# Performance work log

Hardware: AMD Instinct MI355X
Metric: run time of the kernel (lower is better)

The kernel has to match this reference:

```python
import jax, jax.numpy as jnp
import numpy as np

ROPE_THETA = 10000.0
NUM_HEADS = 16


def _apply_rope(t, positions):
    # t: [B, H, S, dh]; positions: [S] int
    dh = t.shape[-1]
    inv_freq = 1.0 / (ROPE_THETA ** (jnp.arange(0, dh, 2, dtype=jnp.float32) / dh))  # [dh/2]
    ang = positions.astype(jnp.float32)[:, None] * inv_freq[None, :]  # [S, dh/2]
    cos = jnp.cos(ang)[None, None]  # [1,1,S,dh/2]
    sin = jnp.sin(ang)[None, None]
    t1 = t[..., 0::2]
    t2 = t[..., 1::2]
    r1 = t1 * cos - t2 * sin
    r2 = t1 * sin + t2 * cos
    # interleave back: (r1_0, r2_0, r1_1, r2_1, ...)
    return jnp.stack([r1, r2], axis=-1).reshape(t.shape)


def setup_inputs() -> dict:
    key = jax.random.key(0)
    ks = jax.random.split(key, 5)
    B, S, D = 4, 2048, 1024
    sigma = np.sqrt(2.0 / (D + D))
    return {
        "x": jax.random.normal(ks[0], (B, S, D), dtype=jnp.float32),
        "WQ": jax.random.normal(ks[1], (D, D), dtype=jnp.float32) * sigma,
        "WK": jax.random.normal(ks[2], (D, D), dtype=jnp.float32) * sigma,
        "WV": jax.random.normal(ks[3], (D, D), dtype=jnp.float32) * sigma,
        "WO": jax.random.normal(ks[4], (D, D), dtype=jnp.float32) * sigma,
        "token_positions": jnp.arange(S, dtype=jnp.int32),
    }


def reference(x, WQ, WK, WV, WO, token_positions):
    B, S, D = x.shape
    H = NUM_HEADS
    dh = D // H

    def proj(W):
        # x @ W.T, then split heads -> [B, H, S, dh]
        return jnp.einsum('bsd,ed->bse', x, W).reshape(B, S, H, dh).transpose(0, 2, 1, 3)

    Q = _apply_rope(proj(WQ), token_positions)
    K = _apply_rope(proj(WK), token_positions)
    V = proj(WV)

    scale = 1.0 / jnp.sqrt(jnp.asarray(dh, dtype=x.dtype))
    scores = jnp.einsum('bhqd,bhkd->bhqk', Q, K) * scale  # [B,H,S,S]
    causal = jnp.tril(jnp.ones((S, S), dtype=bool))
    scores = jnp.where(causal[None, None], scores, jnp.asarray(-jnp.inf, dtype=scores.dtype))
    attn = jax.nn.softmax(scores, axis=-1)
    out = jnp.einsum('bhqk,bhkd->bhqd', attn, V)  # [B,H,S,dh]
    out = out.transpose(0, 2, 1, 3).reshape(B, S, D)
    return out @ WO.T
```

## Files before the change

kernel.cpp:

```cpp
#include <hip/hip_runtime.h>
#include <hip/hip_bf16.h>
#include <math.h>

constexpr int NB   = 4;
constexpr int SEQ  = 2048;
constexpr int DM   = 1024;
constexpr int NH   = 16;
constexpr int DH2  = 64;
constexpr int NROWS = NB * SEQ;

typedef __attribute__((ext_vector_type(8))) short bf16x8;
typedef __attribute__((ext_vector_type(4))) short bf16x4;
typedef __attribute__((ext_vector_type(4))) float f32x4;

__device__ __forceinline__ unsigned short f2bf(float f) {
  __hip_bfloat16 h = __float2bfloat16(f);
  return *reinterpret_cast<unsigned short*>(&h);
}

__device__ __forceinline__ f32x4 mfma16(bf16x8 a, bf16x8 b, f32x4 c) {
  return __builtin_amdgcn_mfma_f32_16x16x32_bf16(a, b, c, 0, 0, 0);
}

__device__ __forceinline__ f32x4 mfma16k16(bf16x4 a, bf16x4 b, f32x4 c) {
  asm("v_mfma_f32_16x16x16_bf16 %0, %1, %2, %0" : "+v"(c) : "v"(a), "v"(b));
  return c;
}

__device__ __forceinline__ void gload_lds16(const void* g, void* l) {
  __builtin_amdgcn_global_load_lds(
      (const __attribute__((address_space(1))) void*)g,
      (__attribute__((address_space(3))) void*)l, 16, 0, 0);
}

__global__ void cast_kernel(const float* __restrict__ in,
                            unsigned short* __restrict__ out, int n4) {
  int i = blockIdx.x * blockDim.x + threadIdx.x;
  int stride = gridDim.x * blockDim.x;
  for (int idx = i; idx < n4; idx += stride) {
    float4 v = reinterpret_cast<const float4*>(in)[idx];
    ushort4 o;
    o.x = f2bf(v.x); o.y = f2bf(v.y); o.z = f2bf(v.z); o.w = f2bf(v.w);
    reinterpret_cast<ushort4*>(out)[idx] = o;
  }
}

__global__ void cast4_kernel(const float* __restrict__ w0, const float* __restrict__ w1,
                             const float* __restrict__ w2, const float* __restrict__ w3,
                             unsigned short* __restrict__ out) {
  constexpr int N4 = DM * DM / 4;
  int idx = blockIdx.x * blockDim.x + threadIdx.x;
  if (idx >= N4) return;
  const float* ins[4] = {w0, w1, w2, w3};
#pragma unroll
  for (int wi = 0; wi < 4; ++wi) {
    float4 v = reinterpret_cast<const float4*>(ins[wi])[idx];
    ushort4 o;
    o.x = f2bf(v.x); o.y = f2bf(v.y); o.z = f2bf(v.z); o.w = f2bf(v.w);
    reinterpret_cast<ushort4*>(out + (size_t)wi * DM * DM)[idx] = o;
  }
}

__global__ void rope_table_kernel(float2* __restrict__ tab, const int* __restrict__ pos) {
  int idx = blockIdx.x * blockDim.x + threadIdx.x;
  if (idx >= SEQ * 32) return;
  int s = idx >> 5, i = idx & 31;
  float inv = powf(10000.0f, -(float)i * (1.0f / 32.0f));
  float ang = (float)pos[s] * inv;
  tab[idx] = make_float2(cosf(ang), sinf(ang));
}

template<int MODE>
__global__ __launch_bounds__(256)
void gemm_bt(const unsigned short* __restrict__ Ag,
             const unsigned short* __restrict__ Bg,
             void* __restrict__ Cout,
             const float2* __restrict__ tab)
{
  constexpr int K = DM;
  __shared__ unsigned short As[128 * 32];
  __shared__ unsigned short Bs[128 * 32];
  const int tid = threadIdx.x;
  const int w = tid >> 6, lane = tid & 63;
  const int wr = w >> 1, wc = w & 1;
  const int r = lane & 15, g = lane >> 4;
  const int rowTile = blockIdx.x, colTile = blockIdx.y;
  const unsigned short* Abase = Ag + (size_t)rowTile * 128 * K;
  const unsigned short* Bbase = Bg + (size_t)colTile * 128 * K;

  f32x4 acc[4][4];
#pragma unroll
  for (int m = 0; m < 4; ++m)
#pragma unroll
    for (int n = 0; n < 4; ++n) acc[m][n] = f32x4{0.f, 0.f, 0.f, 0.f};

  const int e0 = w * 1024 + lane * 8;

  for (int k0 = 0; k0 < K; k0 += 32) {
#pragma unroll
    for (int c = 0; c < 2; ++c) {
      int e = e0 + c * 512;
      int trow = e >> 5, tcol = e & 31;
      gload_lds16(Abase + (size_t)trow * K + k0 + tcol, As + (w * 2 + c) * 512);
      gload_lds16(Bbase + (size_t)trow * K + k0 + tcol, Bs + (w * 2 + c) * 512);
    }
    __syncthreads();
    bf16x8 a[4], b[4];
#pragma unroll
    for (int m = 0; m < 4; ++m)
      a[m] = *reinterpret_cast<const bf16x8*>(As + (wr * 64 + m * 16 + r) * 32 + g * 8);
#pragma unroll
    for (int n = 0; n < 4; ++n)
      b[n] = *reinterpret_cast<const bf16x8*>(Bs + (wc * 64 + n * 16 + r) * 32 + g * 8);
#pragma unroll
    for (int m = 0; m < 4; ++m)
#pragma unroll
      for (int n = 0; n < 4; ++n)
        acc[m][n] = mfma16(a[m], b[n], acc[m][n]);
    __syncthreads();
  }

  const int row0 = rowTile * 128 + wr * 64;
  const int col0 = colTile * 128 + wc * 64;
  if constexpr (MODE == 0) {
    float* C = reinterpret_cast<float*>(Cout);
#pragma unroll
    for (int m = 0; m < 4; ++m)
#pragma unroll
      for (int n = 0; n < 4; ++n)
#pragma unroll
        for (int j = 0; j < 4; ++j) {
          int rr = row0 + m * 16 + g * 4 + j;
          int cc = col0 + n * 16 + r;
          C[(size_t)rr * DM + cc] = acc[m][n][j];
        }
  } else {
    unsigned short* Ob = reinterpret_cast<unsigned short*>(Cout);
#pragma unroll
    for (int m = 0; m < 4; ++m)
#pragma unroll
      for (int n = 0; n < 4; ++n)
#pragma unroll
        for (int j = 0; j < 4; ++j) {
          int rr = row0 + m * 16 + g * 4 + j;
          int ee = col0 + n * 16 + r;
          float val = acc[m][n][j];
          if constexpr (MODE == 1) {
            float partner = __shfl_xor(val, 1);
            int dd = ee & 63;
            int sr = rr & (SEQ - 1);
            float2 cs = tab[sr * 32 + (dd >> 1)];
            val = val * cs.x + (((ee & 1) == 0) ? -partner : partner) * cs.y;
          }
          int bb = rr >> 11;
          int sr2 = rr & (SEQ - 1);
          int h = ee >> 6, d = ee & 63;
          Ob[((size_t)(bb * NH + h) * SEQ + sr2) * DH2 + d] = f2bf(val);
        }
  }
}

__global__ __launch_bounds__(256)
void flash_attn(const unsigned short* __restrict__ Qb,
                const unsigned short* __restrict__ Kb,
                const unsigned short* __restrict__ Vb,
                unsigned short* __restrict__ AO)
{
  constexpr int VST = 68;
  __shared__ unsigned short Vt[2][64 * VST];
  const int tid = threadIdx.x;
  const int w = tid >> 6, lane = tid & 63;
  const int r = lane & 15, g = lane >> 4;
  const int pr = blockIdx.x;
  const int bh = blockIdx.y;
  const unsigned short* Qh = Qb + (size_t)bh * SEQ * DH2;
  const unsigned short* Kh = Kb + (size_t)bh * SEQ * DH2;
  const unsigned short* Vh = Vb + (size_t)bh * SEQ * DH2;
  const int bb = bh >> 4, h = bh & 15;
  const int vd  = (lane & 7) * 8;
  const int vkv = w * 16 + (lane >> 3) * 2;
  const float C = 0.18033688f;
  const float M0 = 11.5415603f;
  const float NEG_INF = -__builtin_inff();

  for (int ctx = 0; ctx < 2; ++ctx) {
    const int qt = ctx ? pr : (15 - pr);
    const int q0w = qt * 128 + w * 32;
    const int nT  = 2 * qt + 2;
    const int myT = 2 * qt + 1 + (w >> 1);

    bf16x8 qf[2][2];
#pragma unroll
    for (int mq = 0; mq < 2; ++mq)
#pragma unroll
      for (int kk = 0; kk < 2; ++kk)
        qf[mq][kk] = *reinterpret_cast<const bf16x8*>(
            Qh + (size_t)(q0w + mq * 16 + r) * DH2 + kk * 32 + g * 8);

    bf16x8 kc[2][4], kn[2][4];
#pragma unroll
    for (int kk = 0; kk < 2; ++kk)
#pragma unroll
      for (int nk = 0; nk < 4; ++nk)
        kc[kk][nk] = *reinterpret_cast<const bf16x8*>(
            Kh + (size_t)(nk * 16 + r) * DH2 + kk * 32 + g * 8);

    {
      uint4 a0 = *reinterpret_cast<const uint4*>(Vh + (size_t)vkv * DH2 + vd);
      uint4 a1 = *reinterpret_cast<const uint4*>(Vh + (size_t)(vkv + 1) * DH2 + vd);
      const unsigned int* d0 = reinterpret_cast<const unsigned int*>(&a0);
      const unsigned int* d1 = reinterpret_cast<const unsigned int*>(&a1);
#pragma unroll
      for (int k2 = 0; k2 < 4; ++k2) {
        *reinterpret_cast<unsigned int*>(&Vt[0][(vd + 2 * k2) * VST + vkv]) =
            __builtin_amdgcn_perm(d1[k2], d0[k2], 0x05040100u);
        *reinterpret_cast<unsigned int*>(&Vt[0][(vd + 2 * k2 + 1) * VST + vkv]) =
            __builtin_amdgcn_perm(d1[k2], d0[k2], 0x07060302u);
      }
    }
    __syncthreads();

    f32x4 oacc[2][4];
    float l_part[2];
#pragma unroll
    for (int mq = 0; mq < 2; ++mq) {
#pragma unroll
      for (int nd = 0; nd < 4; ++nd) oacc[mq][nd] = f32x4{0.f, 0.f, 0.f, 0.f};
      l_part[mq] = 0.f;
    }

    uint4 va0, va1;
    for (int t = 0; t < nT; ++t) {
      const int cur = t & 1;
      const int tn = (t + 1 < nT) ? (t + 1) : t;
      const size_t kv0n = (size_t)tn * 64;

#pragma unroll
      for (int kk = 0; kk < 2; ++kk)
#pragma unroll
        for (int nk = 0; nk < 4; ++nk)
          kn[kk][nk] = *reinterpret_cast<const bf16x8*>(
              Kh + (kv0n + nk * 16 + r) * DH2 + kk * 32 + g * 8);
      va0 = *reinterpret_cast<const uint4*>(Vh + (kv0n + vkv) * DH2 + vd);
      va1 = *reinterpret_cast<const uint4*>(Vh + (kv0n + vkv + 1) * DH2 + vd);

      if (t < myT) {
        const int kv0 = t * 64;
        f32x4 sacc[2][4];
#pragma unroll
        for (int mq = 0; mq < 2; ++mq)
#pragma unroll
          for (int nk = 0; nk < 4; ++nk) sacc[mq][nk] = f32x4{0.f, 0.f, 0.f, 0.f};
        __builtin_amdgcn_s_setprio(1);
#pragma unroll
        for (int kk = 0; kk < 2; ++kk)
#pragma unroll
          for (int mq = 0; mq < 2; ++mq)
#pragma unroll
            for (int nk = 0; nk < 4; ++nk)
              sacc[mq][nk] = mfma16(kc[kk][nk], qf[mq][kk], sacc[mq][nk]);
        __builtin_amdgcn_s_setprio(0);

        if (t == myT - 1) {
#pragma unroll
          for (int mq = 0; mq < 2; ++mq) {
            const int qg = q0w + mq * 16 + r;
#pragma unroll
            for (int nk = 0; nk < 4; ++nk)
#pragma unroll
              for (int j = 0; j < 4; ++j) {
                int kg = kv0 + nk * 16 + g * 4 + j;
                if (kg > qg) sacc[mq][nk][j] = NEG_INF;
              }
          }
        }

        bf16x4 pa[2][4];
#pragma unroll
        for (int mq = 0; mq < 2; ++mq) {
          float ls = 0.f;
#pragma unroll
          for (int nk = 0; nk < 4; ++nk) {
            float p0 = __builtin_amdgcn_exp2f(fmaf(sacc[mq][nk][0], C, -M0));
            float p1 = __builtin_amdgcn_exp2f(fmaf(sacc[mq][nk][1], C, -M0));
            float p2 = __builtin_amdgcn_exp2f(fmaf(sacc[mq][nk][2], C, -M0));
            float p3 = __builtin_amdgcn_exp2f(fmaf(sacc[mq][nk][3], C, -M0));
            ls += (p0 + p1) + (p2 + p3);
            pa[mq][nk] = bf16x4{(short)f2bf(p0), (short)f2bf(p1),
                                (short)f2bf(p2), (short)f2bf(p3)};
          }
          l_part[mq] += ls;
        }

        __builtin_amdgcn_s_setprio(1);
#pragma unroll
        for (int nd = 0; nd < 4; ++nd) {
          bf16x4 vb[4];
#pragma unroll
          for (int nk = 0; nk < 4; ++nk)
            vb[nk] = *reinterpret_cast<const bf16x4*>(
                &Vt[cur][(nd * 16 + r) * VST + nk * 16 + 4 * g]);
#pragma unroll
          for (int mq = 0; mq < 2; ++mq)
#pragma unroll
            for (int nk = 0; nk < 4; ++nk)
              oacc[mq][nd] = mfma16k16(pa[mq][nk], vb[nk], oacc[mq][nd]);
        }
        __builtin_amdgcn_s_setprio(0);
      }

      {
        const unsigned int* d0 = reinterpret_cast<const unsigned int*>(&va0);
        const unsigned int* d1 = reinterpret_cast<const unsigned int*>(&va1);
#pragma unroll
        for (int k2 = 0; k2 < 4; ++k2) {
          *reinterpret_cast<unsigned int*>(&Vt[cur ^ 1][(vd + 2 * k2) * VST + vkv]) =
              __builtin_amdgcn_perm(d1[k2], d0[k2], 0x05040100u);
          *reinterpret_cast<unsigned int*>(&Vt[cur ^ 1][(vd + 2 * k2 + 1) * VST + vkv]) =
              __builtin_amdgcn_perm(d1[k2], d0[k2], 0x07060302u);
        }
      }
#pragma unroll
      for (int kk = 0; kk < 2; ++kk)
#pragma unroll
        for (int nk = 0; nk < 4; ++nk) kc[kk][nk] = kn[kk][nk];
      __syncthreads();
    }

#pragma unroll
    for (int mq = 0; mq < 2; ++mq) {
      float l = l_part[mq];
      l += __shfl_xor(l, 16);
      l += __shfl_xor(l, 32);
#pragma unroll
      for (int j = 0; j < 4; ++j) {
        float inv = 1.0f / __shfl(l, g * 4 + j);
        int srow = q0w + mq * 16 + g * 4 + j;
#pragma unroll
        for (int nd = 0; nd < 4; ++nd) {
          int d = nd * 16 + r;
          AO[(size_t)(bb * SEQ + srow) * DM + h * DH2 + d] = f2bf(oacc[mq][nd][j] * inv);
        }
      }
    }
  }
}

extern "C" void kernel_launch(void* const* d_in, const int* in_sizes, int n_in,
                              void* d_out, int out_size, void* d_ws, size_t ws_size,
                              hipStream_t stream) {
  const float* x  = (const float*)d_in[0];
  const float* WQ = (const float*)d_in[1];
  const float* WK = (const float*)d_in[2];
  const float* WV = (const float*)d_in[3];
  const float* WO = (const float*)d_in[4];
  const int* pos  = (const int*)d_in[5];

  char* ws = (char*)d_ws;
  unsigned short* xb  = (unsigned short*)(ws + 0);
  unsigned short* wqb = (unsigned short*)(ws + (16u << 20));
  unsigned short* wkb = (unsigned short*)(ws + (18u << 20));
  unsigned short* wvb = (unsigned short*)(ws + (20u << 20));
  unsigned short* wob = (unsigned short*)(ws + (22u << 20));
  unsigned short* Qb  = (unsigned short*)(ws + (24u << 20));
  unsigned short* Kb  = (unsigned short*)(ws + (40u << 20));
  unsigned short* Vb  = (unsigned short*)(ws + (56u << 20));
  unsigned short* AO  = (unsigned short*)(ws + (72u << 20));
  float2* tab = (float2*)(ws + (88u << 20));

  cast_kernel<<<2048, 256, 0, stream>>>(x, xb, NROWS * DM / 4);
  cast4_kernel<<<DM * DM / 4 / 256, 256, 0, stream>>>(WQ, WK, WV, WO, wqb);
  rope_table_kernel<<<(SEQ * 32 + 255) / 256, 256, 0, stream>>>(tab, pos);

  dim3 gproj(NROWS / 128, DM / 128);
  gemm_bt<1><<<gproj, 256, 0, stream>>>(xb, wqb, (void*)Qb, tab);
  gemm_bt<1><<<gproj, 256, 0, stream>>>(xb, wkb, (void*)Kb, tab);
  gemm_bt<2><<<gproj, 256, 0, stream>>>(xb, wvb, (void*)Vb, nullptr);
  flash_attn<<<dim3(8, NB * NH), 256, 0, stream>>>(Qb, Kb, Vb, AO);
  gemm_bt<0><<<gproj, 256, 0, stream>>>(AO, wob, d_out, nullptr);
}
```

Baseline: 204.2 us.

## Stage K tiles in shared memory via direct global-to-LDS loads

Instead of each wave loading the full K tile from global memory into registers (redundantly across 4 waves), the block cooperatively loads each K tile into a double-buffered, XOR-swizzled shared buffer using direct global-to-LDS loads, then each wave reads its fragments from LDS. This cuts redundant global/L2 traffic and register pressure from the kc/kn prefetch arrays. It adds LDS reads per iteration, more shared memory per block, and relies on the existing barrier for the async load to complete.

```diff
diff --git a/kernel.cpp b/kernel.cpp
--- a/kernel.cpp
+++ b/kernel.cpp
@@ -167,6 +167,7 @@
                 unsigned short* __restrict__ AO)
 {
   constexpr int VST = 68;
+  __shared__ unsigned short Kl[2 * 64 * 64];
   __shared__ unsigned short Vt[2][64 * VST];
   const int tid = threadIdx.x;
   const int w = tid >> 6, lane = tid & 63;
@@ -183,6 +184,12 @@
   const float M0 = 11.5415603f;
   const float NEG_INF = -__builtin_inff();
 
+  const int krow   = tid >> 3;
+  const int kcol16 = (tid & 7) ^ (krow & 7);
+  const int kgoff  = krow * 64 + kcol16 * 8;
+  const int kread0 = r * 64 + ((g ^ (r & 7)) * 8);
+  const int kread1 = r * 64 + (((4 ^ g) ^ (r & 7)) * 8);
+
   for (int ctx = 0; ctx < 2; ++ctx) {
     const int qt = ctx ? pr : (15 - pr);
     const int q0w = qt * 128 + w * 32;
@@ -197,14 +204,8 @@
         qf[mq][kk] = *reinterpret_cast<const bf16x8*>(
             Qh + (size_t)(q0w + mq * 16 + r) * DH2 + kk * 32 + g * 8);
 
-    bf16x8 kc[2][4], kn[2][4];
-#pragma unroll
-    for (int kk = 0; kk < 2; ++kk)
-#pragma unroll
-      for (int nk = 0; nk < 4; ++nk)
-        kc[kk][nk] = *reinterpret_cast<const bf16x8*>(
-            Kh + (size_t)(nk * 16 + r) * DH2 + kk * 32 + g * 8);
-
+    gload_lds16(Kh + kgoff, Kl + w * 512);
+    gload_lds16(Kh + kgoff + 2048, Kl + 2048 + w * 512);
     {
       uint4 a0 = *reinterpret_cast<const uint4*>(Vh + (size_t)vkv * DH2 + vd);
       uint4 a1 = *reinterpret_cast<const uint4*>(Vh + (size_t)(vkv + 1) * DH2 + vd);
@@ -232,20 +233,26 @@
     uint4 va0, va1;
     for (int t = 0; t < nT; ++t) {
       const int cur = t & 1;
-      const int tn = (t + 1 < nT) ? (t + 1) : t;
-      const size_t kv0n = (size_t)tn * 64;
-
-#pragma unroll
-      for (int kk = 0; kk < 2; ++kk)
-#pragma unroll
-        for (int nk = 0; nk < 4; ++nk)
-          kn[kk][nk] = *reinterpret_cast<const bf16x8*>(
-              Kh + (kv0n + nk * 16 + r) * DH2 + kk * 32 + g * 8);
-      va0 = *reinterpret_cast<const uint4*>(Vh + (kv0n + vkv) * DH2 + vd);
-      va1 = *reinterpret_cast<const uint4*>(Vh + (kv0n + vkv + 1) * DH2 + vd);
+      const unsigned short* Klp = Kl + (cur ? 4096 : 0);
+      unsigned short* Kln = Kl + (cur ? 0 : 4096);
+      const bool haveNext = (t + 1 < nT);
+
+      if (haveNext) {
+        const size_t kv0n = (size_t)(t + 1) * 64;
+        gload_lds16(Kh + kv0n * 64 + kgoff, Kln + w * 512);
+        gload_lds16(Kh + kv0n * 64 + kgoff + 2048, Kln + 2048 + w * 512);
+        va0 = *reinterpret_cast<const uint4*>(Vh + (kv0n + vkv) * DH2 + vd);
+        va1 = *reinterpret_cast<const uint4*>(Vh + (kv0n + vkv + 1) * DH2 + vd);
+      }
 
       if (t < myT) {
         const int kv0 = t * 64;
+        bf16x8 kf0[4], kf1[4];
+#pragma unroll
+        for (int nk = 0; nk < 4; ++nk) {
+          kf0[nk] = *reinterpret_cast<const bf16x8*>(Klp + kread0 + nk * 1024);
+          kf1[nk] = *reinterpret_cast<const bf16x8*>(Klp + kread1 + nk * 1024);
+        }
         f32x4 sacc[2][4];
 #pragma unroll
         for (int mq = 0; mq < 2; ++mq)
@@ -253,12 +260,15 @@
           for (int nk = 0; nk < 4; ++nk) sacc[mq][nk] = f32x4{0.f, 0.f, 0.f, 0.f};
         __builtin_amdgcn_s_setprio(1);
 #pragma unroll
-        for (int kk = 0; kk < 2; ++kk)
-#pragma unroll
-          for (int mq = 0; mq < 2; ++mq)
-#pragma unroll
-            for (int nk = 0; nk < 4; ++nk)
-              sacc[mq][nk] = mfma16(kc[kk][nk], qf[mq][kk], sacc[mq][nk]);
+        for (int mq = 0; mq < 2; ++mq)
+#pragma unroll
+          for (int nk = 0; nk < 4; ++nk)
+            sacc[mq][nk] = mfma16(kf0[nk], qf[mq][0], sacc[mq][nk]);
+#pragma unroll
+        for (int mq = 0; mq < 2; ++mq)
+#pragma unroll
+          for (int nk = 0; nk < 4; ++nk)
+            sacc[mq][nk] = mfma16(kf1[nk], qf[mq][1], sacc[mq][nk]);
         __builtin_amdgcn_s_setprio(0);
 
         if (t == myT - 1) {
@@ -309,7 +319,7 @@
         __builtin_amdgcn_s_setprio(0);
       }
 
-      {
+      if (haveNext) {
         const unsigned int* d0 = reinterpret_cast<const unsigned int*>(&va0);
         const unsigned int* d1 = reinterpret_cast<const unsigned int*>(&va1);
 #pragma unroll
@@ -320,10 +330,6 @@
               __builtin_amdgcn_perm(d1[k2], d0[k2], 0x07060302u);
         }
       }
-#pragma unroll
-      for (int kk = 0; kk < 2; ++kk)
-#pragma unroll
-        for (int nk = 0; nk < 4; ++nk) kc[kk][nk] = kn[kk][nk];
       __syncthreads();
     }
 
```

Result: faster. 195.7 us (median of 2 runs) (-4.2%).
